# Optimization experiments

Hardware: AMD Instinct MI355X
Metric: run time of the kernel (lower is better)

The kernel has to match this reference:

```python
import jax, jax.numpy as jnp
import numpy as np

B, C1, C2, H, W = 4, 128, 256, 128, 128
K, S = 3, 1
N = K * K  # num sampled points = 9
BN_EPS = 1e-5


def setup_inputs() -> dict:
    key = jax.random.key(0)
    ks = jax.random.split(key, 8)
    x = jax.random.normal(ks[0], (B, C1, H, W), jnp.float32)
    # offset-prediction conv: 3x3, stride S, pad 1, out channels 2*N
    w_off = jax.random.normal(ks[1], (2 * N, C1, 3, 3), jnp.float32) * 0.01
    b_off = jnp.zeros((2 * N,), jnp.float32)
    # main conv over the N sampled points: equivalent to Conv2d(C1,C2,(N,1),stride=(N,1),bias=None)
    w_main = jax.random.normal(ks[2], (C2, C1, N), jnp.float32) * (1.0 / np.sqrt(C1 * N))
    bn_gamma = jax.random.uniform(ks[3], (C2,), jnp.float32, 0.5, 1.5)
    bn_beta = jax.random.normal(ks[4], (C2,), jnp.float32) * 0.1
    bn_mean = jax.random.normal(ks[5], (C2,), jnp.float32) * 0.1
    bn_var = jax.random.uniform(ks[6], (C2,), jnp.float32, 0.5, 1.5)
    return dict(x=x, w_off=w_off, b_off=b_off, w_main=w_main,
                bn_gamma=bn_gamma, bn_beta=bn_beta, bn_mean=bn_mean, bn_var=bn_var)


def _grid_pn():
    # base kernel sampling grid for N points: round(sqrt(N)) x base grid, values 0..base-1
    base = int(round(np.sqrt(N)))
    px, py = np.meshgrid(np.arange(base), np.arange(base), indexing='ij')
    return jnp.asarray(px.reshape(-1), jnp.float32), jnp.asarray(py.reshape(-1), jnp.float32)


def _akconv_forward(x, w_off, b_off, w_main, bn_gamma, bn_beta, bn_mean, bn_var):
    # offset prediction: (b, 2N, h, w)
    offset = jax.lax.conv_general_dilated(
        x, w_off, (S, S), ((1, 1), (1, 1)),
        dimension_numbers=('NCHW', 'OIHW', 'NCHW')) + b_off[None, :, None, None]
    b, _, h, w = offset.shape
    off_x = offset[:, :N].transpose(0, 2, 3, 1)   # (b,h,w,N) row offsets
    off_y = offset[:, N:].transpose(0, 2, 3, 1)   # (b,h,w,N) col offsets
    pn_x, pn_y = _grid_pn()
    p0_x = (jnp.arange(h, dtype=jnp.float32) * S)[None, :, None, None]
    p0_y = (jnp.arange(w, dtype=jnp.float32) * S)[None, None, :, None]
    px = jnp.clip(off_x + pn_x[None, None, None, :] + p0_x, 0.0, H - 1.0)
    py = jnp.clip(off_y + pn_y[None, None, None, :] + p0_y, 0.0, W - 1.0)
    x0 = jnp.clip(jnp.floor(px), 0.0, H - 1.0)
    y0 = jnp.clip(jnp.floor(py), 0.0, W - 1.0)
    x1 = jnp.clip(x0 + 1.0, 0.0, H - 1.0)
    y1 = jnp.clip(y0 + 1.0, 0.0, W - 1.0)
    # bilinear weights (official AKConv formulation)
    g_lt = (1.0 + (x0 - px)) * (1.0 + (y0 - py))
    g_rb = (1.0 - (x1 - px)) * (1.0 - (y1 - py))
    g_lb = (1.0 + (x0 - px)) * (1.0 - (y1 - py))
    g_rt = (1.0 - (x1 - px)) * (1.0 + (y0 - py))
    xf = x.reshape(b, C1, H * W)

    def gather(qx, qy):
        idx = (qx * W + qy).astype(jnp.int32).reshape(b, 1, h * w * N)
        g = jnp.take_along_axis(xf, jnp.broadcast_to(idx, (b, C1, h * w * N)), axis=2)
        return g.reshape(b, C1, h, w, N)

    # fused bilinear combine: (b, C1, h, w, N)
    x_off = (g_lt[:, None] * gather(x0, y0)
             + g_rb[:, None] * gather(x1, y1)
             + g_lb[:, None] * gather(x0, y1)
             + g_rt[:, None] * gather(x1, y0))
    # main conv over sampled points == Conv2d(kernel=(N,1), stride=(N,1)) on rearranged tensor
    out = jnp.einsum('bchwn,ocn->bohw', x_off, w_main)
    # inference-mode BatchNorm
    inv = bn_gamma / jnp.sqrt(bn_var + BN_EPS)
    out = out * inv[None, :, None, None] + (bn_beta - bn_mean * inv)[None, :, None, None]
    # wrapper SiLU activation
    return jax.nn.silu(out)


def reference(x, w_off, b_off, w_main, bn_gamma, bn_beta, bn_mean, bn_var):
    return _akconv_forward(x, w_off, b_off, w_main, bn_gamma, bn_beta, bn_mean, bn_var)
```

## Files before the change

kernel.cpp:

```cpp
#include <hip/hip_runtime.h>
#include <math.h>

typedef __attribute__((ext_vector_type(8))) short short8;
typedef __attribute__((ext_vector_type(4))) float f32x4;
typedef __attribute__((ext_vector_type(4))) uint  uint4v;
typedef __attribute__((ext_vector_type(4))) int   int4v;

#define BB  4
#define C1  128
#define C2  256
#define HH  128
#define WW  128
#define NPT 9
#define HWN (HH*WW)

#define XT_OFF    0ull
#define WB3_OFF   16777216ull
#define WOF32_OFF (WB3_OFF + 589824ull)
#define BN_OFF    (WOF32_OFF + 82944ull)
#define OFFP_OFF  (BN_OFF + 2048ull)
#define PART_OFF  (OFFP_OFF + 4718592ull)
#define WS_FUSED_NEED (PART_OFF + 18874368ull)

__device__ __forceinline__ ushort f2bf(float f) {
  uint u = __builtin_bit_cast(uint, f);
  u += 0x7FFFu + ((u >> 16) & 1u);
  return (ushort)(u >> 16);
}
__device__ __forceinline__ float u2f(uint u) {
  return __builtin_bit_cast(float, u);
}

__global__ __launch_bounds__(256) void prep(
    const float* __restrict__ w_main, const float* __restrict__ w_off,
    const float* __restrict__ g, const float* __restrict__ be,
    const float* __restrict__ mu, const float* __restrict__ var,
    ushort* ws_u, float* ws_f) {
  int t = blockIdx.x * 256 + threadIdx.x;
  if (t < C1 * NPT * C2) {
    int j = t & 7, lane = (t >> 3) & 63, kc = (t >> 9) & 3;
    int ob = (t >> 11) & 15, n = t >> 15;
    int o = ob * 16 + (lane & 15);
    int c = kc * 32 + (lane >> 4) * 8 + j;
    ws_u[WB3_OFF / 2 + t] = f2bf(w_main[(o * C1 + c) * NPT + n]);
  } else if (t < C1 * NPT * C2 + 128 * 2 * 81) {
    int e = t - C1 * NPT * C2;
    int c2 = e / 81, r81 = e - c2 * 81;
    int q = c2 & 1, c = c2 >> 1;
    int tap = r81 / 9, i = r81 - tap * 9;
    int oc = q * 9 + i;
    ws_f[WOF32_OFF / 4 + e] = w_off[(oc * C1 + c) * 9 + tap];
  } else if (t < C1 * NPT * C2 + 128 * 2 * 81 + C2) {
    int o = t - (C1 * NPT * C2 + 128 * 2 * 81);
    float inv = g[o] * rsqrtf(var[o] + 1e-5f);
    ws_f[BN_OFF / 4 + o] = inv;
    ws_f[BN_OFF / 4 + 256 + o] = be[o] - mu[o] * inv;
  }
}

__global__ __launch_bounds__(256) void stage1(
    const float* __restrict__ x, const float* __restrict__ b_off,
    const float* __restrict__ ws_f_ro, ushort* ws_u, float* __restrict__ part) {
  __shared__ __align__(16) ushort tile[32][68];
  int blk = blockIdx.x;
  int tid = threadIdx.x;

  if (blk < 4 * BB * HH) {
    int cg = blk & 3, bh = blk >> 2;
    int h = bh & 127, b = bh >> 7;
    int w = tid & 127, q = tid >> 7;
    int qu = __builtin_amdgcn_readfirstlane(q);
    const float* wq = ws_f_ro + WOF32_OFF / 4 + qu * 81;
    const float* xb = x + ((size_t)b * C1 + cg * 32) * HWN;

    float acc[9];
#pragma unroll
    for (int i = 0; i < 9; ++i) acc[i] = (cg == 0) ? b_off[qu * 9 + i] : 0.f;

    int hc0 = (h >= 1) ? h - 1 : 0, hc2 = (h < 127) ? h + 1 : 127;
    int wc0 = (w >= 1) ? w - 1 : 0, wc2 = (w < 127) ? w + 1 : 127;
    bool vh0 = (h >= 1), vh2 = (h < 127);
    bool vw0 = (w >= 1), vw2 = (w < 127);
    int o[9];
    o[0] = hc0 * 128 + wc0; o[1] = hc0 * 128 + w; o[2] = hc0 * 128 + wc2;
    o[3] = h   * 128 + wc0; o[4] = h   * 128 + w; o[5] = h   * 128 + wc2;
    o[6] = hc2 * 128 + wc0; o[7] = hc2 * 128 + w; o[8] = hc2 * 128 + wc2;
    bool vm[9];
    vm[0] = vh0 && vw0; vm[1] = vh0; vm[2] = vh0 && vw2;
    vm[3] = vw0;        vm[4] = true; vm[5] = vw2;
    vm[6] = vh2 && vw0; vm[7] = vh2; vm[8] = vh2 && vw2;

    for (int ci = 0; ci < 32; ++ci) {
      const float* xc = xb + (size_t)ci * HWN;
      float xv[9];
#pragma unroll
      for (int k = 0; k < 9; ++k) {
        float rr = xc[o[k]];
        xv[k] = vm[k] ? rr : 0.f;
      }
      const float* wp = wq + (cg * 32 + ci) * 162;
#pragma unroll
      for (int tap = 0; tap < 9; ++tap)
#pragma unroll
        for (int i = 0; i < 9; ++i)
          acc[i] = fmaf(xv[tap], wp[tap * 9 + i], acc[i]);
    }
    int pos = (b * HH + h) * WW + w;
#pragma unroll
    for (int i = 0; i < 9; ++i)
      part[(size_t)(cg * 18 + qu * 9 + i) * 65536 + pos] = acc[i];
  } else {
    int bid = blk - 4 * BB * HH;
    int wt = bid & 1, h = (bid >> 1) & 127, cb = (bid >> 8) & 3, b = bid >> 10;
    int c0 = cb * 32, w0 = wt * 64;
    int wl = tid & 63, rr = tid >> 6;
#pragma unroll
    for (int it = 0; it < 8; ++it) {
      int ci = it * 4 + rr;
      tile[ci][wl] = f2bf(x[(((size_t)b * C1 + c0 + ci) * HWN) + h * WW + w0 + wl]);
    }
    __syncthreads();
    int wl2 = tid >> 2, cg = tid & 3;
    short8 pk;
#pragma unroll
    for (int k = 0; k < 8; ++k) pk[k] = (short)tile[cg * 8 + k][wl2];
    *(short8*)(ws_u + XT_OFF / 2 +
               (((size_t)(b * HH + h) * WW + w0 + wl2) * C1 + c0 + cg * 8)) = pk;
  }
}

__global__ __launch_bounds__(256) void off_reduce_soa(
    const float* __restrict__ part, float* __restrict__ ws_f) {
  int e = blockIdx.x * 256 + threadIdx.x;
  int oc = e >> 16, pos = e & 65535;
  float s = part[(size_t)oc * 65536 + pos]
          + part[(size_t)(18 + oc) * 65536 + pos]
          + part[(size_t)(36 + oc) * 65536 + pos]
          + part[(size_t)(54 + oc) * 65536 + pos];
  ws_f[OFFP_OFF / 4 + (size_t)oc * 65536 + pos] = s;
}

#define ALDS_STRIDE 136
__global__ __launch_bounds__(1024, 8) void akconv_main_mfma16(
    const ushort* ws_u, const float* ws_f, float* out, int fused) {
  __shared__ __align__(16) int4v sidx[576];
  __shared__ __align__(16) f32x4 swgt[576];
  __shared__ __align__(16) ushort alds[2][64 * ALDS_STRIDE];

  int tid = threadIdx.x;
  int blk = blockIdx.x;
  int xcd = blk & 7, idx = blk >> 3;
  int b  = xcd >> 1;
  int h  = ((xcd & 1) << 6) + (idx >> 1);
  int wt = idx & 1;
  int w0 = wt * 64;

  if (tid < 576) {
    int n = tid >> 6, wl = tid & 63;
    int pos = (b * HH + h) * WW + w0 + wl;
    float ox, oy;
    if (fused) {
      const float* pp = ws_f + PART_OFF / 4;
      ox = pp[(size_t)n * 65536 + pos]
         + pp[(size_t)(18 + n) * 65536 + pos]
         + pp[(size_t)(36 + n) * 65536 + pos]
         + pp[(size_t)(54 + n) * 65536 + pos];
      oy = pp[(size_t)(9 + n) * 65536 + pos]
         + pp[(size_t)(27 + n) * 65536 + pos]
         + pp[(size_t)(45 + n) * 65536 + pos]
         + pp[(size_t)(63 + n) * 65536 + pos];
    } else {
      const float* offp = ws_f + OFFP_OFF / 4;
      ox = offp[(size_t)n * 65536 + pos];
      oy = offp[(size_t)(9 + n) * 65536 + pos];
    }
    float px = ox + (float)(n / 3) + (float)h;
    float py = oy + (float)(n - (n / 3) * 3) + (float)(w0 + wl);
    px = fminf(fmaxf(px, 0.f), 127.f);
    py = fminf(fmaxf(py, 0.f), 127.f);
    float x0 = floorf(px), y0 = floorf(py);
    float x1 = fminf(x0 + 1.f, 127.f), y1 = fminf(y0 + 1.f, 127.f);
    f32x4 g;
    g[0] = (1.f + (x0 - px)) * (1.f + (y0 - py));
    g[1] = (1.f - (x1 - px)) * (1.f - (y1 - py));
    g[2] = (1.f + (x0 - px)) * (1.f - (y1 - py));
    g[3] = (1.f - (x1 - px)) * (1.f + (y0 - py));
    int ix0 = (int)x0, iy0 = (int)y0, ix1 = (int)x1, iy1 = (int)y1;
    int4v iv;
    iv[0] = (ix0 * WW + iy0) << 8;
    iv[1] = (ix1 * WW + iy1) << 8;
    iv[2] = (ix0 * WW + iy1) << 8;
    iv[3] = (ix1 * WW + iy0) << 8;
    sidx[tid] = iv;
    swgt[tid] = g;
  }

  const char* xTb = (const char*)ws_u + (size_t)b * (HWN * 256);
  const ushort* wB3 = ws_u + WB3_OFF / 2;
  int lane = tid & 63, r = lane & 15, kg = lane >> 4;
  int wv = __builtin_amdgcn_readfirstlane(tid >> 6);

  int p   = tid >> 4;
  int oct = tid & 15;
  int coff = oct * 16;
  int wr = p * ALDS_STRIDE + oct * 8;

  f32x4 acc[4];
#pragma unroll
  for (int mi = 0; mi < 4; ++mi) acc[mi] = (f32x4)0.0f;

  __syncthreads();

  uint4v gv[4];
  f32x4 gw;

#define GLOAD(nn)                                                       \
  {                                                                     \
    int e = (nn) * 64 + p;                                              \
    int4v iv = sidx[e];                                                 \
    gw = swgt[e];                                                       \
    gv[0] = *(const uint4v*)(xTb + iv[0] + coff);                       \
    gv[1] = *(const uint4v*)(xTb + iv[1] + coff);                       \
    gv[2] = *(const uint4v*)(xTb + iv[2] + coff);                       \
    gv[3] = *(const uint4v*)(xTb + iv[3] + coff);                       \
  }

#define GCOMBINE(bufb)                                                  \
  {                                                                     \
    uint4v pkv;                                                         \
    _Pragma("unroll")                                                   \
    for (int jj = 0; jj < 4; ++jj) {                                    \
      float flo = gw[0] * u2f(gv[0][jj] << 16) + gw[1] * u2f(gv[1][jj] << 16) \
                + gw[2] * u2f(gv[2][jj] << 16) + gw[3] * u2f(gv[3][jj] << 16);\
      float fhi = gw[0] * u2f(gv[0][jj] & 0xffff0000u)                  \
                + gw[1] * u2f(gv[1][jj] & 0xffff0000u)                  \
                + gw[2] * u2f(gv[2][jj] & 0xffff0000u)                  \
                + gw[3] * u2f(gv[3][jj] & 0xffff0000u);                 \
      uint upk;                                                         \
      asm("v_cvt_pk_bf16_f32 %0, %1, %2" : "=v"(upk) : "v"(flo), "v"(fhi)); \
      pkv[jj] = upk;                                                    \
    }                                                                   \
    *(uint4v*)(&alds[bufb][wr]) = pkv;                                  \
  }

  GLOAD(0);
  GCOMBINE(0);
  __syncthreads();

  for (int n = 0; n < 9; ++n) {
    int buf = n & 1;
    if (n < 8) GLOAD(n + 1);
#pragma unroll
    for (int kc = 0; kc < 4; ++kc) {
      short8 bfrag = *(const short8*)(wB3 +
          (((size_t)(n * 16 + wv) * 4 + kc) * 64 + lane) * 8);
#pragma unroll
      for (int mi = 0; mi < 4; ++mi) {
        short8 a = *(const short8*)(&alds[buf][(mi * 16 + r) * ALDS_STRIDE + (kc * 4 + kg) * 8]);
        acc[mi] = __builtin_amdgcn_mfma_f32_16x16x32_bf16(bfrag, a, acc[mi], 0, 0, 0);
      }
    }
    if (n < 8) GCOMBINE(buf ^ 1);
    __syncthreads();
  }
#undef GLOAD
#undef GCOMBINE

  const float* bnA = ws_f + BN_OFF / 4;
  const float* bnB = bnA + 256;
  int ob = wv * 16 + kg * 4;
#pragma unroll
  for (int j = 0; j < 4; ++j) {
    int o = ob + j;
    float sA = bnA[o], sB = bnB[o];
#pragma unroll
    for (int mi = 0; mi < 4; ++mi) {
      float v = acc[mi][j] * sA + sB;
      float sv = v / (1.f + __expf(-v));
      out[(((size_t)b * C2 + o) * HWN) + h * WW + w0 + mi * 16 + r] = sv;
    }
  }
}

extern "C" void kernel_launch(void* const* d_in, const int* in_sizes, int n_in,
                              void* d_out, int out_size, void* d_ws, size_t ws_size,
                              hipStream_t stream) {
  const float* x        = (const float*)d_in[0];
  const float* w_off    = (const float*)d_in[1];
  const float* b_off    = (const float*)d_in[2];
  const float* w_main   = (const float*)d_in[3];
  const float* bn_gamma = (const float*)d_in[4];
  const float* bn_beta  = (const float*)d_in[5];
  const float* bn_mean  = (const float*)d_in[6];
  const float* bn_var   = (const float*)d_in[7];
  ushort* ws_u = (ushort*)d_ws;
  float*  ws_f = (float*)d_ws;
  float*  out  = (float*)d_out;

  int fused = (ws_size >= WS_FUSED_NEED) ? 1 : 0;
  float* part_dst = fused ? (ws_f + PART_OFF / 4) : out;

  int prep_tasks = C1 * NPT * C2 + 128 * 2 * 81 + C2;
  prep<<<(prep_tasks + 255) / 256, 256, 0, stream>>>(
      w_main, w_off, bn_gamma, bn_beta, bn_mean, bn_var, ws_u, ws_f);
  stage1<<<4 * BB * HH + BB * 4 * HH * 2, 256, 0, stream>>>(
      x, b_off, ws_f, ws_u, part_dst);
  if (!fused) {
    off_reduce_soa<<<(18 * 65536) / 256, 256, 0, stream>>>(out, ws_f);
  }
  akconv_main_mfma16<<<BB * HH * 2, 1024, 0, stream>>>(ws_u, ws_f, out, fused);
}
```

Measured before the change: 138.2 us.

## Fold weight prep into stage1 and read offset-conv weights directly with packed FMA

Removes the separate prep kernel launch by appending its work (bf16 main-weight repacking and BN folding) as extra blocks of stage1. The offset-conv weight reordering is dropped, so stage1 reads w_off in its original layout and accumulates with 2-wide float vectors so the compiler can emit packed FMA. This saves one launch and one dependency barrier. The cost is less coalesced, uniform weight reads and a summation order that differs slightly from before.

```diff
diff --git a/kernel.cpp b/kernel.cpp
--- a/kernel.cpp
+++ b/kernel.cpp
@@ -3,6 +3,7 @@
 
 typedef __attribute__((ext_vector_type(8))) short short8;
 typedef __attribute__((ext_vector_type(4))) float f32x4;
+typedef __attribute__((ext_vector_type(2))) float f32x2;
 typedef __attribute__((ext_vector_type(4))) uint  uint4v;
 typedef __attribute__((ext_vector_type(4))) int   int4v;
 
@@ -16,11 +17,14 @@
 
 #define XT_OFF    0ull
 #define WB3_OFF   16777216ull
-#define WOF32_OFF (WB3_OFF + 589824ull)
-#define BN_OFF    (WOF32_OFF + 82944ull)
+#define BN_OFF    (WB3_OFF + 589824ull)
 #define OFFP_OFF  (BN_OFF + 2048ull)
 #define PART_OFF  (OFFP_OFF + 4718592ull)
 #define WS_FUSED_NEED (PART_OFF + 18874368ull)
+
+#define NB_OFF  (4 * BB * HH)
+#define NB_TR   (BB * 4 * HH * 2)
+#define NB_PREP 1153
 
 __device__ __forceinline__ ushort f2bf(float f) {
   uint u = __builtin_bit_cast(uint, f);
@@ -31,51 +35,31 @@
   return __builtin_bit_cast(float, u);
 }
 
-__global__ __launch_bounds__(256) void prep(
-    const float* __restrict__ w_main, const float* __restrict__ w_off,
+__global__ __launch_bounds__(256) void stage1(
+    const float* __restrict__ x, const float* __restrict__ b_off,
+    const float* __restrict__ w_off, const float* __restrict__ w_main,
     const float* __restrict__ g, const float* __restrict__ be,
     const float* __restrict__ mu, const float* __restrict__ var,
-    ushort* ws_u, float* ws_f) {
-  int t = blockIdx.x * 256 + threadIdx.x;
-  if (t < C1 * NPT * C2) {
-    int j = t & 7, lane = (t >> 3) & 63, kc = (t >> 9) & 3;
-    int ob = (t >> 11) & 15, n = t >> 15;
-    int o = ob * 16 + (lane & 15);
-    int c = kc * 32 + (lane >> 4) * 8 + j;
-    ws_u[WB3_OFF / 2 + t] = f2bf(w_main[(o * C1 + c) * NPT + n]);
-  } else if (t < C1 * NPT * C2 + 128 * 2 * 81) {
-    int e = t - C1 * NPT * C2;
-    int c2 = e / 81, r81 = e - c2 * 81;
-    int q = c2 & 1, c = c2 >> 1;
-    int tap = r81 / 9, i = r81 - tap * 9;
-    int oc = q * 9 + i;
-    ws_f[WOF32_OFF / 4 + e] = w_off[(oc * C1 + c) * 9 + tap];
-  } else if (t < C1 * NPT * C2 + 128 * 2 * 81 + C2) {
-    int o = t - (C1 * NPT * C2 + 128 * 2 * 81);
-    float inv = g[o] * rsqrtf(var[o] + 1e-5f);
-    ws_f[BN_OFF / 4 + o] = inv;
-    ws_f[BN_OFF / 4 + 256 + o] = be[o] - mu[o] * inv;
-  }
-}
-
-__global__ __launch_bounds__(256) void stage1(
-    const float* __restrict__ x, const float* __restrict__ b_off,
-    const float* __restrict__ ws_f_ro, ushort* ws_u, float* __restrict__ part) {
+    ushort* ws_u, float* ws_f, float* __restrict__ part) {
   __shared__ __align__(16) ushort tile[32][68];
   int blk = blockIdx.x;
   int tid = threadIdx.x;
 
-  if (blk < 4 * BB * HH) {
+  if (blk < NB_OFF) {
     int cg = blk & 3, bh = blk >> 2;
     int h = bh & 127, b = bh >> 7;
     int w = tid & 127, q = tid >> 7;
     int qu = __builtin_amdgcn_readfirstlane(q);
-    const float* wq = ws_f_ro + WOF32_OFF / 4 + qu * 81;
+    int quoff = qu * 9;
     const float* xb = x + ((size_t)b * C1 + cg * 32) * HWN;
 
-    float acc[9];
-#pragma unroll
-    for (int i = 0; i < 9; ++i) acc[i] = (cg == 0) ? b_off[qu * 9 + i] : 0.f;
+    f32x2 acc2[9];
+    float accs[9];
+#pragma unroll
+    for (int i = 0; i < 9; ++i) {
+      acc2[i] = (f32x2)0.0f;
+      accs[i] = (cg == 0) ? b_off[quoff + i] : 0.f;
+    }
 
     int hc0 = (h >= 1) ? h - 1 : 0, hc2 = (h < 127) ? h + 1 : 127;
     int wc0 = (w >= 1) ? w - 1 : 0, wc2 = (w < 127) ? w + 1 : 127;
@@ -91,6 +75,7 @@
     vm[6] = vh2 && vw0; vm[7] = vh2; vm[8] = vh2 && vw2;
 
     for (int ci = 0; ci < 32; ++ci) {
+      int c = cg * 32 + ci;
       const float* xc = xb + (size_t)ci * HWN;
       float xv[9];
 #pragma unroll
@@ -98,19 +83,28 @@
         float rr = xc[o[k]];
         xv[k] = vm[k] ? rr : 0.f;
       }
-      const float* wp = wq + (cg * 32 + ci) * 162;
-#pragma unroll
-      for (int tap = 0; tap < 9; ++tap)
-#pragma unroll
-        for (int i = 0; i < 9; ++i)
-          acc[i] = fmaf(xv[tap], wp[tap * 9 + i], acc[i]);
+      f32x2 xp0 = {xv[0], xv[1]}, xp1 = {xv[2], xv[3]};
+      f32x2 xp2 = {xv[4], xv[5]}, xp3 = {xv[6], xv[7]};
+      float x8 = xv[8];
+#pragma unroll
+      for (int i = 0; i < 9; ++i) {
+        const float* wp = w_off + ((size_t)(quoff + i) * C1 + c) * 9;
+        f32x2 w01 = {wp[0], wp[1]}, w23 = {wp[2], wp[3]};
+        f32x2 w45 = {wp[4], wp[5]}, w67 = {wp[6], wp[7]};
+        acc2[i] = xp0 * w01 + acc2[i];
+        acc2[i] = xp1 * w23 + acc2[i];
+        acc2[i] = xp2 * w45 + acc2[i];
+        acc2[i] = xp3 * w67 + acc2[i];
+        accs[i] = fmaf(x8, wp[8], accs[i]);
+      }
     }
     int pos = (b * HH + h) * WW + w;
 #pragma unroll
     for (int i = 0; i < 9; ++i)
-      part[(size_t)(cg * 18 + qu * 9 + i) * 65536 + pos] = acc[i];
-  } else {
-    int bid = blk - 4 * BB * HH;
+      part[(size_t)(cg * 18 + quoff + i) * 65536 + pos] = acc2[i][0] + acc2[i][1] + accs[i];
+
+  } else if (blk < NB_OFF + NB_TR) {
+    int bid = blk - NB_OFF;
     int wt = bid & 1, h = (bid >> 1) & 127, cb = (bid >> 8) & 3, b = bid >> 10;
     int c0 = cb * 32, w0 = wt * 64;
     int wl = tid & 63, rr = tid >> 6;
@@ -126,6 +120,21 @@
     for (int k = 0; k < 8; ++k) pk[k] = (short)tile[cg * 8 + k][wl2];
     *(short8*)(ws_u + XT_OFF / 2 +
                (((size_t)(b * HH + h) * WW + w0 + wl2) * C1 + c0 + cg * 8)) = pk;
+
+  } else {
+    int t = (blk - NB_OFF - NB_TR) * 256 + tid;
+    if (t < C1 * NPT * C2) {
+      int j = t & 7, lane = (t >> 3) & 63, kc = (t >> 9) & 3;
+      int ob = (t >> 11) & 15, n = t >> 15;
+      int o = ob * 16 + (lane & 15);
+      int c = kc * 32 + (lane >> 4) * 8 + j;
+      ws_u[WB3_OFF / 2 + t] = f2bf(w_main[(o * C1 + c) * NPT + n]);
+    } else {
+      int o = t - C1 * NPT * C2;
+      float inv = g[o] * rsqrtf(var[o] + 1e-5f);
+      ws_f[BN_OFF / 4 + o] = inv;
+      ws_f[BN_OFF / 4 + 256 + o] = be[o] - mu[o] * inv;
+    }
   }
 }
 
@@ -300,11 +309,9 @@
   int fused = (ws_size >= WS_FUSED_NEED) ? 1 : 0;
   float* part_dst = fused ? (ws_f + PART_OFF / 4) : out;
 
-  int prep_tasks = C1 * NPT * C2 + 128 * 2 * 81 + C2;
-  prep<<<(prep_tasks + 255) / 256, 256, 0, stream>>>(
-      w_main, w_off, bn_gamma, bn_beta, bn_mean, bn_var, ws_u, ws_f);
-  stage1<<<4 * BB * HH + BB * 4 * HH * 2, 256, 0, stream>>>(
-      x, b_off, ws_f, ws_u, part_dst);
+  stage1<<<NB_OFF + NB_TR + NB_PREP, 256, 0, stream>>>(
+      x, b_off, w_off, w_main, bn_gamma, bn_beta, bn_mean, bn_var,
+      ws_u, ws_f, part_dst);
   if (!fused) {
     off_reduce_soa<<<(18 * 65536) / 256, 256, 0, stream>>>(out, ws_f);
   }
```

New measurement: 132.0 us (median of 2 runs). 1.05x faster.
